# Optimization experiments

Hardware: AMD Instinct MI355X
Metric: run time of the kernel (lower is better)

## Reference

```python
import jax, jax.numpy as jnp
import numpy as np

B, TD, SD, H = 512, 2048, 768, 128


def setup_inputs() -> dict:
    key = jax.random.key(0)
    ks = jax.random.split(key, 12)
    s = lambda k, shape, fan_in: jax.random.normal(k, shape, jnp.float32) * (1.0 / np.sqrt(fan_in))
    return {
        "teacher_features": jax.random.normal(ks[0], (B, TD), jnp.float32),
        "student_features": jax.random.normal(ks[1], (B, SD), jnp.float32),
        # Linear weights stored [in, out] (transposed vs torch) so y = x @ W + b
        "Wt": s(ks[2], (TD, H), TD), "bt": jnp.zeros((H,), jnp.float32),
        "Ws": s(ks[3], (SD, H), SD), "bs": jnp.zeros((H,), jnp.float32),
        "W1": s(ks[4], (2 * H, H), 2 * H), "b1": jnp.zeros((H,), jnp.float32),
        "W2": s(ks[5], (H, 1), H), "b2": jnp.zeros((1,), jnp.float32),
    }


def reference(teacher_features, student_features, Wt, bt, Ws, bs, W1, b1, W2, b2):
    def compute_relations(f):
        b, h = f.shape
        # pairwise concat [f_i, f_j] -> [B, B, 2H]
        pair = jnp.concatenate(
            [jnp.broadcast_to(f[:, None, :], (b, b, h)),
             jnp.broadcast_to(f[None, :, :], (b, b, h))], axis=-1)
        hdn = jax.nn.relu(jnp.einsum('ijk,kh->ijh', pair, W1) + b1)
        rel = jax.nn.sigmoid(jnp.einsum('ijh,ho->ijo', hdn, W2) + b2)[..., 0]
        # diagonal stays zero (i != j in the original loop)
        return rel * (1.0 - jnp.eye(b, dtype=rel.dtype))

    tp = teacher_features @ Wt + bt  # [B, H]
    sp = student_features @ Ws + bs  # [B, H]
    t_rel = compute_relations(tp)
    s_rel = compute_relations(sp)
    return jnp.mean((s_rel - t_rel) ** 2)
```

## Files before the change

### kernel.cpp

```cpp
#include <hip/hip_runtime.h>

#define HDIM 128
#define BDIM 512

typedef __attribute__((ext_vector_type(8))) __bf16 bf16x8;
typedef __attribute__((ext_vector_type(4))) float  f32x4;

__global__ __launch_bounds__(256) void proj_mfma(
    const float* __restrict__ Ft, const float* __restrict__ Fs,
    const float* __restrict__ Wt, const float* __restrict__ Ws,
    __bf16* __restrict__ Pbt, __bf16* __restrict__ Pbs)
{
    const int tid = threadIdx.x;
    const int wv = tid >> 6, l = tid & 63;
    const int t = blockIdx.x;
    const int net = t >> 8;
    const int mtile = (t >> 3) & 31, ntile = t & 7;

    const float* F; const float* W; __bf16* P; int K;
    if (net == 0) { F = Ft; W = Wt; P = Pbt; K = 2048; }
    else          { F = Fs; W = Ws; P = Pbs; K = 768;  }

    const int m0 = mtile * 16, n0 = ntile * 16;
    const int Ks = K >> 2;
    const int q = l >> 4, ln = l & 15;
    const int arow = m0 + ln;
    const int bn = n0 + ln;

    f32x4 acc = {0.f, 0.f, 0.f, 0.f};
    for (int k0 = wv * Ks; k0 < (wv + 1) * Ks; k0 += 32) {
        const int ka = k0 + q * 8;
        const float4 fa0 = *(const float4*)&F[(size_t)arow * K + ka];
        const float4 fa1 = *(const float4*)&F[(size_t)arow * K + ka + 4];
        bf16x8 a, b;
        a[0] = (__bf16)fa0.x; a[1] = (__bf16)fa0.y; a[2] = (__bf16)fa0.z; a[3] = (__bf16)fa0.w;
        a[4] = (__bf16)fa1.x; a[5] = (__bf16)fa1.y; a[6] = (__bf16)fa1.z; a[7] = (__bf16)fa1.w;
        #pragma unroll
        for (int j = 0; j < 8; ++j)
            b[j] = (__bf16)W[(size_t)(ka + j) * HDIM + bn];
        acc = __builtin_amdgcn_mfma_f32_16x16x32_bf16(a, b, acc, 0, 0, 0);
    }

    __shared__ float lds[4 * 256];
    #pragma unroll
    for (int r = 0; r < 4; ++r) lds[wv * 256 + r * 64 + l] = acc[r];
    __syncthreads();

    {
        const float s = lds[tid] + lds[256 + tid] + lds[512 + tid] + lds[768 + tid];
        const int r = tid >> 6, l2 = tid & 63;
        const int row = m0 + ((l2 >> 4) << 2) + r;
        const int col = n0 + (l2 & 15);
        P[(size_t)row * HDIM + col] = (__bf16)s;
    }
}

__global__ __launch_bounds__(64) void uv_mfma(
    const __bf16* __restrict__ Pbt, const __bf16* __restrict__ Pbs,
    const float* __restrict__ bt, const float* __restrict__ bs,
    const float* __restrict__ W1, const float* __restrict__ b1,
    float* __restrict__ Ut, float* __restrict__ Vt,
    float* __restrict__ Us, float* __restrict__ Vs,
    float* __restrict__ out)
{
    const int t = blockIdx.x;
    const int net = t >> 9, uvh = (t >> 8) & 1;
    const int mtile = (t >> 3) & 31, ntile = t & 7;
    const int l = threadIdx.x;

    if (t == 0 && l == 0) out[0] = 0.f;

    const __bf16* P   = net ? Pbs : Pbt;
    const float* bias = net ? bs : bt;
    float* O = net ? (uvh ? Vs : Us) : (uvh ? Vt : Ut);
    const float* W1o = W1 + (size_t)uvh * HDIM * HDIM;

    const int m0 = mtile * 16, n0 = ntile * 16;
    const int q = l >> 4, ln = l & 15;
    const int arow = m0 + ln, bn = n0 + ln;

    f32x4 acc = {0.f, 0.f, 0.f, 0.f};
    float cpart = 0.f;
    #pragma unroll
    for (int k0 = 0; k0 < HDIM; k0 += 32) {
        const int ka = k0 + q * 8;
        bf16x8 a = *(const bf16x8*)&P[(size_t)arow * HDIM + ka];
        bf16x8 b;
        #pragma unroll
        for (int j = 0; j < 8; ++j) {
            const float w = W1o[(size_t)(ka + j) * HDIM + bn];
            b[j] = (__bf16)w;
            cpart = fmaf(bias[ka + j], w, cpart);
        }
        acc = __builtin_amdgcn_mfma_f32_16x16x32_bf16(a, b, acc, 0, 0, 0);
    }
    cpart += __shfl_xor(cpart, 16, 64);
    cpart += __shfl_xor(cpart, 32, 64);
    const float cfull = cpart + (uvh == 0 ? b1[bn] : 0.f);

    #pragma unroll
    for (int r = 0; r < 4; ++r) {
        const int row = m0 + q * 4 + r;
        O[(size_t)row * HDIM + bn] = acc[r] + cfull;
    }
}

__global__ __launch_bounds__(256) void pair_kernel(
    const float* __restrict__ Ut, const float* __restrict__ Vt,
    const float* __restrict__ Us, const float* __restrict__ Vs,
    const float* __restrict__ W2, const float* __restrict__ b2,
    float* __restrict__ out)
{
    __shared__ alignas(16) float4 tUt[32 * 17];
    __shared__ alignas(16) float4 tVt[32 * 17];
    __shared__ alignas(16) float4 tUs[32 * 17];
    __shared__ alignas(16) float4 tVs[32 * 17];
    __shared__ alignas(16) float4 w2s[32];
    __shared__ float red[256];

    const int tx = threadIdx.x, ty = threadIdx.y;
    const int tid = ty * 16 + tx;
    const int i0 = blockIdx.y * 32, j0 = blockIdx.x * 32;

    const float4* Ut4 = (const float4*)Ut;
    const float4* Vt4 = (const float4*)Vt;
    const float4* Us4 = (const float4*)Us;
    const float4* Vs4 = (const float4*)Vs;

    if (tid < 32) w2s[tid] = ((const float4*)W2)[tid];

    float aT[2][2] = {{0.f, 0.f}, {0.f, 0.f}};
    float aS[2][2] = {{0.f, 0.f}, {0.f, 0.f}};

    for (int half = 0; half < 2; ++half) {
        const int c0 = half * 16;
        __syncthreads();
        #pragma unroll
        for (int it = 0; it < 2; ++it) {
            int fi = tid + 256 * it;
            int r = fi >> 4, c = fi & 15;
            tUt[r * 17 + c] = Ut4[(size_t)(i0 + r) * 32 + c0 + c];
            tVt[r * 17 + c] = Vt4[(size_t)(j0 + r) * 32 + c0 + c];
            tUs[r * 17 + c] = Us4[(size_t)(i0 + r) * 32 + c0 + c];
            tVs[r * 17 + c] = Vs4[(size_t)(j0 + r) * 32 + c0 + c];
        }
        __syncthreads();

        #pragma unroll 4
        for (int h4 = 0; h4 < 16; ++h4) {
            float4 w = w2s[c0 + h4];
            float4 u[2], v[2], p[2], q[2];
            u[0] = tUt[ty * 17 + h4];        u[1] = tUt[(ty + 16) * 17 + h4];
            v[0] = tVt[tx * 17 + h4];        v[1] = tVt[(tx + 16) * 17 + h4];
            p[0] = tUs[ty * 17 + h4];        p[1] = tUs[(ty + 16) * 17 + h4];
            q[0] = tVs[tx * 17 + h4];        q[1] = tVs[(tx + 16) * 17 + h4];
            #pragma unroll
            for (int a = 0; a < 2; ++a)
                #pragma unroll
                for (int b = 0; b < 2; ++b) {
                    aT[a][b] = fmaf(fmaxf(u[a].x + v[b].x, 0.f), w.x,
                               fmaf(fmaxf(u[a].y + v[b].y, 0.f), w.y,
                               fmaf(fmaxf(u[a].z + v[b].z, 0.f), w.z,
                               fmaf(fmaxf(u[a].w + v[b].w, 0.f), w.w, aT[a][b]))));
                    aS[a][b] = fmaf(fmaxf(p[a].x + q[b].x, 0.f), w.x,
                               fmaf(fmaxf(p[a].y + q[b].y, 0.f), w.y,
                               fmaf(fmaxf(p[a].z + q[b].z, 0.f), w.z,
                               fmaf(fmaxf(p[a].w + q[b].w, 0.f), w.w, aS[a][b]))));
                }
        }
    }

    const float b2v = b2[0];
    float local = 0.f;
    #pragma unroll
    for (int a = 0; a < 2; ++a)
        #pragma unroll
        for (int b = 0; b < 2; ++b) {
            int i = i0 + ty + 16 * a;
            int j = j0 + tx + 16 * b;
            if (i != j) {
                float tr = 1.f / (1.f + __expf(-(aT[a][b] + b2v)));
                float sr = 1.f / (1.f + __expf(-(aS[a][b] + b2v)));
                float d = sr - tr;
                local = fmaf(d, d, local);
            }
        }

    red[tid] = local;
    __syncthreads();
    #pragma unroll
    for (int s = 128; s > 0; s >>= 1) {
        if (tid < s) red[tid] += red[tid + s];
        __syncthreads();
    }
    if (tid == 0)
        atomicAdd(out, red[0] * (1.0f / ((float)BDIM * (float)BDIM)));
}

extern "C" void kernel_launch(void* const* d_in, const int* in_sizes, int n_in,
                              void* d_out, int out_size, void* d_ws, size_t ws_size,
                              hipStream_t stream) {
    const float* teacher = (const float*)d_in[0];
    const float* student = (const float*)d_in[1];
    const float* Wt = (const float*)d_in[2];
    const float* bt = (const float*)d_in[3];
    const float* Ws = (const float*)d_in[4];
    const float* bs = (const float*)d_in[5];
    const float* W1 = (const float*)d_in[6];
    const float* b1 = (const float*)d_in[7];
    const float* W2 = (const float*)d_in[8];
    const float* b2 = (const float*)d_in[9];
    float* out = (float*)d_out;

    const size_t M = (size_t)BDIM * HDIM;
    __bf16* Pbt = (__bf16*)d_ws;
    __bf16* Pbs = Pbt + M;
    float* Ut = (float*)(Pbs + M);
    float* Vt = Ut + M;
    float* Us = Vt + M;
    float* Vs = Us + M;

    proj_mfma<<<512, 256, 0, stream>>>(teacher, student, Wt, Ws, Pbt, Pbs);

    uv_mfma<<<1024, 64, 0, stream>>>(Pbt, Pbs, bt, bs, W1, b1,
                                     Ut, Vt, Us, Vs, out);

    pair_kernel<<<dim3(16, 16), dim3(16, 16), 0, stream>>>(
        Ut, Vt, Us, Vs, W2, b2, out);
}
```

Measured before the change: 98.56 us.

## Store U/V in bf16 and use packed f32x2 math in pair kernel

The intermediate U/V projections are now written as bf16 instead of fp32, which halves their global traffic and lets the whole 128-wide tile fit in LDS in a single load with one barrier. The pair kernel unpacks bf16 pairs to float2 and accumulates with two-wide vector add/max/mul, aiming for packed FP32 instructions, and reads W2 straight from global memory instead of LDS. This costs precision in the pairwise hidden activations and adds unpack shift/mask work in the inner loop.

```diff
diff --git a/kernel.cpp b/kernel.cpp
--- a/kernel.cpp
+++ b/kernel.cpp
@@ -5,6 +5,7 @@
 
 typedef __attribute__((ext_vector_type(8))) __bf16 bf16x8;
 typedef __attribute__((ext_vector_type(4))) float  f32x4;
+typedef __attribute__((ext_vector_type(2))) float  f32x2;
 
 __global__ __launch_bounds__(256) void proj_mfma(
     const float* __restrict__ Ft, const float* __restrict__ Fs,
@@ -45,7 +46,6 @@
     #pragma unroll
     for (int r = 0; r < 4; ++r) lds[wv * 256 + r * 64 + l] = acc[r];
     __syncthreads();
-
     {
         const float s = lds[tid] + lds[256 + tid] + lds[512 + tid] + lds[768 + tid];
         const int r = tid >> 6, l2 = tid & 63;
@@ -59,8 +59,8 @@
     const __bf16* __restrict__ Pbt, const __bf16* __restrict__ Pbs,
     const float* __restrict__ bt, const float* __restrict__ bs,
     const float* __restrict__ W1, const float* __restrict__ b1,
-    float* __restrict__ Ut, float* __restrict__ Vt,
-    float* __restrict__ Us, float* __restrict__ Vs,
+    __bf16* __restrict__ Ut, __bf16* __restrict__ Vt,
+    __bf16* __restrict__ Us, __bf16* __restrict__ Vs,
     float* __restrict__ out)
 {
     const int t = blockIdx.x;
@@ -72,7 +72,7 @@
 
     const __bf16* P   = net ? Pbs : Pbt;
     const float* bias = net ? bs : bt;
-    float* O = net ? (uvh ? Vs : Us) : (uvh ? Vt : Ut);
+    __bf16* O = net ? (uvh ? Vs : Us) : (uvh ? Vt : Ut);
     const float* W1o = W1 + (size_t)uvh * HDIM * HDIM;
 
     const int m0 = mtile * 16, n0 = ntile * 16;
@@ -101,71 +101,75 @@
     #pragma unroll
     for (int r = 0; r < 4; ++r) {
         const int row = m0 + q * 4 + r;
-        O[(size_t)row * HDIM + bn] = acc[r] + cfull;
-    }
+        O[(size_t)row * HDIM + bn] = (__bf16)(acc[r] + cfull);
+    }
+}
+
+__device__ __forceinline__ f32x2 bf2up(unsigned d) {
+    f32x2 r;
+    r.x = __uint_as_float(d << 16);
+    r.y = __uint_as_float(d & 0xffff0000u);
+    return r;
 }
 
 __global__ __launch_bounds__(256) void pair_kernel(
-    const float* __restrict__ Ut, const float* __restrict__ Vt,
-    const float* __restrict__ Us, const float* __restrict__ Vs,
+    const __bf16* __restrict__ Ut, const __bf16* __restrict__ Vt,
+    const __bf16* __restrict__ Us, const __bf16* __restrict__ Vs,
     const float* __restrict__ W2, const float* __restrict__ b2,
     float* __restrict__ out)
 {
-    __shared__ alignas(16) float4 tUt[32 * 17];
-    __shared__ alignas(16) float4 tVt[32 * 17];
-    __shared__ alignas(16) float4 tUs[32 * 17];
-    __shared__ alignas(16) float4 tVs[32 * 17];
-    __shared__ alignas(16) float4 w2s[32];
+    __shared__ alignas(16) uint4 tU[2][32 * 17];
+    __shared__ alignas(16) uint4 tV[2][32 * 17];
     __shared__ float red[256];
 
     const int tx = threadIdx.x, ty = threadIdx.y;
     const int tid = ty * 16 + tx;
     const int i0 = blockIdx.y * 32, j0 = blockIdx.x * 32;
 
-    const float4* Ut4 = (const float4*)Ut;
-    const float4* Vt4 = (const float4*)Vt;
-    const float4* Us4 = (const float4*)Us;
-    const float4* Vs4 = (const float4*)Vs;
-
-    if (tid < 32) w2s[tid] = ((const float4*)W2)[tid];
-
-    float aT[2][2] = {{0.f, 0.f}, {0.f, 0.f}};
-    float aS[2][2] = {{0.f, 0.f}, {0.f, 0.f}};
-
-    for (int half = 0; half < 2; ++half) {
-        const int c0 = half * 16;
-        __syncthreads();
-        #pragma unroll
-        for (int it = 0; it < 2; ++it) {
-            int fi = tid + 256 * it;
-            int r = fi >> 4, c = fi & 15;
-            tUt[r * 17 + c] = Ut4[(size_t)(i0 + r) * 32 + c0 + c];
-            tVt[r * 17 + c] = Vt4[(size_t)(j0 + r) * 32 + c0 + c];
-            tUs[r * 17 + c] = Us4[(size_t)(i0 + r) * 32 + c0 + c];
-            tVs[r * 17 + c] = Vs4[(size_t)(j0 + r) * 32 + c0 + c];
-        }
-        __syncthreads();
-
-        #pragma unroll 4
-        for (int h4 = 0; h4 < 16; ++h4) {
-            float4 w = w2s[c0 + h4];
-            float4 u[2], v[2], p[2], q[2];
-            u[0] = tUt[ty * 17 + h4];        u[1] = tUt[(ty + 16) * 17 + h4];
-            v[0] = tVt[tx * 17 + h4];        v[1] = tVt[(tx + 16) * 17 + h4];
-            p[0] = tUs[ty * 17 + h4];        p[1] = tUs[(ty + 16) * 17 + h4];
-            q[0] = tVs[tx * 17 + h4];        q[1] = tVs[(tx + 16) * 17 + h4];
+    const uint4* Ut4 = (const uint4*)Ut;
+    const uint4* Vt4 = (const uint4*)Vt;
+    const uint4* Us4 = (const uint4*)Us;
+    const uint4* Vs4 = (const uint4*)Vs;
+
+    #pragma unroll
+    for (int it = 0; it < 2; ++it) {
+        int fi = tid + 256 * it;
+        int r = fi >> 4, c = fi & 15;
+        tU[0][r * 17 + c] = Ut4[(size_t)(i0 + r) * 16 + c];
+        tU[1][r * 17 + c] = Us4[(size_t)(i0 + r) * 16 + c];
+        tV[0][r * 17 + c] = Vt4[(size_t)(j0 + r) * 16 + c];
+        tV[1][r * 17 + c] = Vs4[(size_t)(j0 + r) * 16 + c];
+    }
+    __syncthreads();
+
+    f32x2 aT[2][2] = {{{0.f,0.f},{0.f,0.f}},{{0.f,0.f},{0.f,0.f}}};
+    f32x2 aS[2][2] = {{{0.f,0.f},{0.f,0.f}},{{0.f,0.f},{0.f,0.f}}};
+    const f32x2 z2 = {0.f, 0.f};
+
+    #pragma unroll 4
+    for (int h8 = 0; h8 < 16; ++h8) {
+        const uint4 u0 = tU[0][ty * 17 + h8], u1 = tU[0][(ty + 16) * 17 + h8];
+        const uint4 v0 = tV[0][tx * 17 + h8], v1 = tV[0][(tx + 16) * 17 + h8];
+        const uint4 p0 = tU[1][ty * 17 + h8], p1 = tU[1][(ty + 16) * 17 + h8];
+        const uint4 q0 = tV[1][tx * 17 + h8], q1 = tV[1][(tx + 16) * 17 + h8];
+        const unsigned ud[2][4] = {{u0.x,u0.y,u0.z,u0.w},{u1.x,u1.y,u1.z,u1.w}};
+        const unsigned vd[2][4] = {{v0.x,v0.y,v0.z,v0.w},{v1.x,v1.y,v1.z,v1.w}};
+        const unsigned pd[2][4] = {{p0.x,p0.y,p0.z,p0.w},{p1.x,p1.y,p1.z,p1.w}};
+        const unsigned qd[2][4] = {{q0.x,q0.y,q0.z,q0.w},{q1.x,q1.y,q1.z,q1.w}};
+        #pragma unroll
+        for (int c = 0; c < 4; ++c) {
+            const f32x2 w = *(const f32x2*)&W2[h8 * 8 + 2 * c];
+            f32x2 U[2], V[2], Pp[2], Q[2];
+            #pragma unroll
+            for (int a = 0; a < 2; ++a) { U[a] = bf2up(ud[a][c]); Pp[a] = bf2up(pd[a][c]); }
+            #pragma unroll
+            for (int b = 0; b < 2; ++b) { V[b] = bf2up(vd[b][c]); Q[b] = bf2up(qd[b][c]); }
             #pragma unroll
             for (int a = 0; a < 2; ++a)
                 #pragma unroll
                 for (int b = 0; b < 2; ++b) {
-                    aT[a][b] = fmaf(fmaxf(u[a].x + v[b].x, 0.f), w.x,
-                               fmaf(fmaxf(u[a].y + v[b].y, 0.f), w.y,
-                               fmaf(fmaxf(u[a].z + v[b].z, 0.f), w.z,
-                               fmaf(fmaxf(u[a].w + v[b].w, 0.f), w.w, aT[a][b]))));
-                    aS[a][b] = fmaf(fmaxf(p[a].x + q[b].x, 0.f), w.x,
-                               fmaf(fmaxf(p[a].y + q[b].y, 0.f), w.y,
-                               fmaf(fmaxf(p[a].z + q[b].z, 0.f), w.z,
-                               fmaf(fmaxf(p[a].w + q[b].w, 0.f), w.w, aS[a][b]))));
+                    aT[a][b] += __builtin_elementwise_max(U[a] + V[b], z2) * w;
+                    aS[a][b] += __builtin_elementwise_max(Pp[a] + Q[b], z2) * w;
                 }
         }
     }
@@ -179,8 +183,10 @@
             int i = i0 + ty + 16 * a;
             int j = j0 + tx + 16 * b;
             if (i != j) {
-                float tr = 1.f / (1.f + __expf(-(aT[a][b] + b2v)));
-                float sr = 1.f / (1.f + __expf(-(aS[a][b] + b2v)));
+                float st = aT[a][b].x + aT[a][b].y;
+                float ss = aS[a][b].x + aS[a][b].y;
+                float tr = 1.f / (1.f + __expf(-(st + b2v)));
+                float sr = 1.f / (1.f + __expf(-(ss + b2v)));
                 float d = sr - tr;
                 local = fmaf(d, d, local);
             }
@@ -215,10 +221,10 @@
     const size_t M = (size_t)BDIM * HDIM;
     __bf16* Pbt = (__bf16*)d_ws;
     __bf16* Pbs = Pbt + M;
-    float* Ut = (float*)(Pbs + M);
-    float* Vt = Ut + M;
-    float* Us = Vt + M;
-    float* Vs = Us + M;
+    __bf16* Ut  = Pbs + M;
+    __bf16* Vt  = Ut + M;
+    __bf16* Us  = Vt + M;
+    __bf16* Vs  = Us + M;
 
     proj_mfma<<<512, 256, 0, stream>>>(teacher, student, Wt, Ws, Pbt, Pbs);
 
```

After: 98.67 us. Within noise of the previous version (+0.1%).
